# Optimization experiments

Hardware: AMD Instinct MI355X
Metric: run time of the kernel (lower is better)

The kernel has to match this reference:

```python
import jax, jax.numpy as jnp
import numpy as np

NUM_HEADS = 16
ROPE_BASE = 10000.0


def _rope_cos_sin(seq_len, head_dim, dtype):
    inv_freq = 1.0 / (ROPE_BASE ** (jnp.arange(0, head_dim, 2, dtype=jnp.float32) / head_dim))
    t = jnp.arange(seq_len, dtype=jnp.float32)
    freqs = jnp.einsum('i,j->ij', t, inv_freq)          # [S, hd/2]
    emb = jnp.concatenate([freqs, freqs], axis=-1)      # [S, hd]
    return jnp.cos(emb).astype(dtype), jnp.sin(emb).astype(dtype)


def _rotate_half(x):
    x1, x2 = jnp.split(x, 2, axis=-1)
    return jnp.concatenate([-x2, x1], axis=-1)


def setup_inputs() -> dict:
    key = jax.random.key(0)
    k1, k2, k3 = jax.random.split(key, 3)
    B, S, D = 2, 2048, 2048
    x = jax.random.normal(k1, (B, S, D), dtype=jnp.float32)
    w_qkv = jax.random.normal(k2, (D, 3 * D), dtype=jnp.float32) * (D ** -0.5)
    w_out = jax.random.normal(k3, (D, D), dtype=jnp.float32) * (D ** -0.5)
    return {"x": x, "w_qkv": w_qkv, "w_out": w_out}


def reference(x, w_qkv, w_out):
    B, S, D = x.shape
    H = NUM_HEADS
    hd = D // H
    scale = hd ** -0.5

    qkv = jnp.einsum('bsd,de->bse', x, w_qkv)            # [B,S,3D]
    q, k, v = jnp.split(qkv, 3, axis=-1)
    # -> [B,H,S,hd]
    q = q.reshape(B, S, H, hd).transpose(0, 2, 1, 3)
    k = k.reshape(B, S, H, hd).transpose(0, 2, 1, 3)
    v = v.reshape(B, S, H, hd).transpose(0, 2, 1, 3)

    cos, sin = _rope_cos_sin(S, hd, x.dtype)             # [S,hd]
    cos = cos[None, None]                                # [1,1,S,hd]
    sin = sin[None, None]
    q = q * cos + _rotate_half(q) * sin
    k = k * cos + _rotate_half(k) * sin

    scores = jnp.einsum('bhqd,bhkd->bhqk', q, k) * scale  # [B,H,S,S]
    attn = jax.nn.softmax(scores, axis=-1)                # non-causal: no mask
    out = jnp.einsum('bhqk,bhkd->bhqd', attn, v)          # [B,H,S,hd]
    out = out.transpose(0, 2, 1, 3).reshape(B, S, D)
    out = jnp.einsum('bsd,de->bse', out, w_out)
    return out
```

## Files before the change

### kernel.cpp

```cpp
#include <hip/hip_runtime.h>
#include <hip/hip_bf16.h>

typedef __hip_bfloat16 bf16_t;
typedef __bf16 bf16x8 __attribute__((ext_vector_type(8)));
typedef float floatx4 __attribute__((ext_vector_type(4)));

#define DEVINL __device__ __forceinline__

DEVINL floatx4 mfma16(bf16x8 a, bf16x8 b, floatx4 c) {
  return __builtin_amdgcn_mfma_f32_16x16x32_bf16(a, b, c, 0, 0, 0);
}

DEVINL void gload_lds16(const bf16_t* gp, bf16_t* lp) {
  __builtin_amdgcn_global_load_lds(
      (const __attribute__((address_space(1))) unsigned int*)gp,
      (__attribute__((address_space(3))) unsigned int*)lp, 16, 0, 0);
}

template <class CT> DEVINL CT cvtC(float f);
template <> DEVINL bf16_t cvtC<bf16_t>(float f) { return __float2bfloat16(f); }
template <> DEVINL float cvtC<float>(float f) { return f; }

DEVINL unsigned int pack_bf2(float a, float b) {
  union { bf16_t h; unsigned short s; } ua, ub;
  ua.h = __float2bfloat16(a);
  ub.h = __float2bfloat16(b);
  return (unsigned int)ua.s | ((unsigned int)ub.s << 16);
}

__global__ void convert_f32_bf16(const float* __restrict__ in,
                                 bf16_t* __restrict__ out) {
  size_t i = ((size_t)blockIdx.x * 256 + threadIdx.x) * 8;
  floatx4 a = *(const floatx4*)(in + i);
  floatx4 b = *(const floatx4*)(in + i + 4);
  bf16x8 r;
#pragma unroll
  for (int j = 0; j < 4; j++) r[j] = (__bf16)a[j];
#pragma unroll
  for (int j = 0; j < 4; j++) r[4 + j] = (__bf16)b[j];
  *(bf16x8*)(out + i) = r;
}

template <bool SPLITV, class CT>
__global__ __launch_bounds__(256, 3) void gemm_bt(
    const bf16_t* __restrict__ A, const bf16_t* __restrict__ BT,
    CT* __restrict__ C, bf16_t* __restrict__ VTout, int M, int N, int CN,
    int K) {
  __shared__ __align__(16) bf16_t a_lds[8 * 1024];
  __shared__ __align__(16) bf16_t b_lds[8 * 1024];

  const int tid = threadIdx.x;
  const int wave = tid >> 6;
  const int lane = tid & 63;
  const int quad = lane >> 4;
  const int l16 = lane & 15;
  const int wm = wave >> 1, wn = wave & 1;

  const int nx = N >> 7;
  const int bid = blockIdx.x;
  const int row0 = ((bid & 7) + 8 * (bid / (8 * nx))) * 128;
  const int col0 = ((bid >> 3) % nx) * 128;

  floatx4 acc[4][4] = {};

  const bf16_t* ag = A + (size_t)(row0 + wave * 32 + l16) * K + quad * 8;
  const bf16_t* bg = BT + (size_t)(col0 + wave * 32 + l16) * K + quad * 8;

  bf16x8 pa[2][2], pb[2][2];
#define LOAD_TILE(k0)                                                       \
  {                                                                         \
    _Pragma("unroll") for (int t = 0; t < 2; t++)                           \
        _Pragma("unroll") for (int kc = 0; kc < 2; kc++) {                  \
      pa[t][kc] = *(const bf16x8*)(ag + (k0) + (size_t)(t * 16) * K + kc * 32); \
      pb[t][kc] = *(const bf16x8*)(bg + (k0) + (size_t)(t * 16) * K + kc * 32); \
    }                                                                       \
  }
#define STORE_TILE()                                                        \
  {                                                                         \
    _Pragma("unroll") for (int t = 0; t < 2; t++)                           \
        _Pragma("unroll") for (int kc = 0; kc < 2; kc++) {                  \
      *(bf16x8*)(a_lds + (wave * 2 + t) * 1024 + kc * 512 + lane * 8) =     \
          pa[t][kc];                                                        \
      *(bf16x8*)(b_lds + (wave * 2 + t) * 1024 + kc * 512 + lane * 8) =     \
          pb[t][kc];                                                        \
    }                                                                       \
  }

  LOAD_TILE(0);
  STORE_TILE();
  __syncthreads();

  for (int k0 = 0; k0 < K; k0 += 64) {
    const bool more = (k0 + 64) < K;
    if (more) LOAD_TILE(k0 + 64);
#pragma unroll
    for (int kc = 0; kc < 2; kc++) {
      bf16x8 af[4], bfr[4];
#pragma unroll
      for (int i = 0; i < 4; i++)
        af[i] = *(const bf16x8*)(a_lds + (wm * 4 + i) * 1024 + kc * 512 +
                                 lane * 8);
#pragma unroll
      for (int j = 0; j < 4; j++)
        bfr[j] = *(const bf16x8*)(b_lds + (wn * 4 + j) * 1024 + kc * 512 +
                                  lane * 8);
#pragma unroll
      for (int i = 0; i < 4; i++)
#pragma unroll
        for (int j = 0; j < 4; j++)
          acc[i][j] = mfma16(af[i], bfr[j], acc[i][j]);
    }
    __syncthreads();
    if (more) STORE_TILE();
    __syncthreads();
  }
#undef LOAD_TILE
#undef STORE_TILE

  if (!SPLITV || col0 < 4096) {
#pragma unroll
    for (int i = 0; i < 4; i++)
#pragma unroll
      for (int j = 0; j < 4; j++)
#pragma unroll
        for (int r = 0; r < 4; r++) {
          int row = row0 + wm * 64 + i * 16 + quad * 4 + r;
          int col = col0 + wn * 64 + j * 16 + l16;
          C[(size_t)row * CN + col] = cvtC<CT>(acc[i][j][r]);
        }
  } else {
    const int h = (col0 - 4096) >> 7;
    const int b = row0 >> 11;
    const int s0 = row0 & 2047;
    bf16_t* vt = VTout + (size_t)(b * 16 + h) * 128 * 2048;
    struct __align__(8) bf4 { bf16_t v[4]; };
#pragma unroll
    for (int i = 0; i < 4; i++)
#pragma unroll
      for (int j = 0; j < 4; j++) {
        int d = wn * 64 + j * 16 + l16;
        int s = s0 + wm * 64 + i * 16 + quad * 4;
        bf4 o;
#pragma unroll
        for (int r = 0; r < 4; r++) o.v[r] = __float2bfloat16(acc[i][j][r]);
        *(bf4*)(vt + (size_t)d * 2048 + s) = o;
      }
  }
}

__global__ void transposecvt(const float* __restrict__ in,
                             bf16_t* __restrict__ out, int M, int N) {
  __shared__ bf16_t tile[32][33];
  int n0 = blockIdx.x * 32, m0 = blockIdx.y * 32;
  tile[threadIdx.y][threadIdx.x] =
      __float2bfloat16(in[(size_t)(m0 + threadIdx.y) * N + n0 + threadIdx.x]);
  __syncthreads();
  out[(size_t)(n0 + threadIdx.y) * M + m0 + threadIdx.x] =
      tile[threadIdx.x][threadIdx.y];
}

__global__ void rope_qk(bf16_t* __restrict__ qkv) {
  struct __align__(8) bf4 { bf16_t v[4]; };
  int t = blockIdx.x * 256 + threadIdx.x;
  int dc = t & 15;
  int s = (t >> 4) & 2047;
  int h = (t >> 15) & 15;
  int b = t >> 19;
  int d = dc * 4;
  size_t base = ((size_t)(b * 2048 + s) * 2) * 2048 + h * 128;
  bf4 ql = *(const bf4*)(qkv + base + d);
  bf4 qh = *(const bf4*)(qkv + base + d + 64);
  bf4 kl = *(const bf4*)(qkv + base + 2048 + d);
  bf4 kh = *(const bf4*)(qkv + base + 2048 + d + 64);
  bf4 oql, oqh, okl, okh;
  const float scale = 0.08838834764831845f;
#pragma unroll
  for (int i = 0; i < 4; i++) {
    int j = d + i;
    float fr = (float)s * exp2f((float)j * -0.20762050593045858f);
    float c, sn;
    __sincosf(fr, &sn, &c);
    float qlo = __bfloat162float(ql.v[i]), qhi = __bfloat162float(qh.v[i]);
    float klo = __bfloat162float(kl.v[i]), khi = __bfloat162float(kh.v[i]);
    oql.v[i] = __float2bfloat16((qlo * c - qhi * sn) * scale);
    oqh.v[i] = __float2bfloat16((qhi * c + qlo * sn) * scale);
    okl.v[i] = __float2bfloat16(klo * c - khi * sn);
    okh.v[i] = __float2bfloat16(khi * c + klo * sn);
  }
  *(bf4*)(qkv + base + d) = oql;
  *(bf4*)(qkv + base + d + 64) = oqh;
  *(bf4*)(qkv + base + 2048 + d) = okl;
  *(bf4*)(qkv + base + 2048 + d + 64) = okh;
}

__global__ __launch_bounds__(256, 2) void flash_attn(
    const bf16_t* __restrict__ qkv, const bf16_t* __restrict__ VT,
    bf16_t* __restrict__ Out) {
  const int S = 2048;
  const int RS = 4096;
  const int tid = threadIdx.x;
  const int wave = tid >> 6;
  const int lane = tid & 63;
  const int quad = lane >> 4;
  const int l16 = lane & 15;

  const int bh = blockIdx.y;
  const int q0 = blockIdx.x * 128;
  const int b = bh >> 4, h = bh & 15;

  const bf16_t* Qb = qkv + (size_t)b * S * RS + h * 128;
  const bf16_t* Kb = Qb + 2048;
  const bf16_t* Vb = VT + (size_t)bh * 128 * S;

  __shared__ __align__(16) bf16_t k_lds[16384];
  __shared__ __align__(16) bf16_t v_lds[16384];

  bf16x8 qf[2][4];
#pragma unroll
  for (int qn = 0; qn < 2; qn++)
#pragma unroll
    for (int ks = 0; ks < 4; ks++)
      qf[qn][ks] = *(const bf16x8*)(
          Qb + (size_t)(q0 + wave * 32 + qn * 16 + l16) * RS + ks * 32 +
          quad * 8);

  floatx4 o_acc[2][8] = {};
  float l_part[2] = {0.f, 0.f};

  const int sA = l16 + 32 * (quad & 1);
  const int sB = sA + 16;
  const bool hi = quad >= 2;

  for (int kt = 0; kt < S / 128; kt++) {
    const int kk0 = kt * 128;
#pragma unroll
    for (int t = 0; t < 2; t++) {
      int mt = wave * 2 + t;
#pragma unroll
      for (int ks = 0; ks < 4; ks++) {
        gload_lds16(Kb + (size_t)(kk0 + mt * 16 + l16) * RS + ks * 32 + quad * 8,
                    k_lds + mt * 2048 + ks * 512);
        gload_lds16(Vb + (size_t)(mt * 16 + l16) * S + kk0 + ks * 32 + quad * 8,
                    v_lds + mt * 2048 + ks * 512);
      }
    }
    __syncthreads();

    floatx4 s_acc[2][8] = {};
    __builtin_amdgcn_s_setprio(1);
#pragma unroll
    for (int ks = 0; ks < 4; ks++)
#pragma unroll
      for (int mt = 0; mt < 8; mt++) {
        bf16x8 kf = *(const bf16x8*)(k_lds + mt * 2048 + ks * 512 + lane * 8);
        s_acc[0][mt] = mfma16(kf, qf[0][ks], s_acc[0][mt]);
        s_acc[1][mt] = mfma16(kf, qf[1][ks], s_acc[1][mt]);
      }
    __builtin_amdgcn_s_setprio(0);

    unsigned int p01[2][8], p23[2][8];
#pragma unroll
    for (int qn = 0; qn < 2; qn++)
#pragma unroll
      for (int mt = 0; mt < 8; mt++) {
        float e0 = __expf(s_acc[qn][mt][0]);
        float e1 = __expf(s_acc[qn][mt][1]);
        float e2 = __expf(s_acc[qn][mt][2]);
        float e3 = __expf(s_acc[qn][mt][3]);
        l_part[qn] += (e0 + e1) + (e2 + e3);
        p01[qn][mt] = pack_bf2(e0, e1);
        p23[qn][mt] = pack_bf2(e2, e3);
      }

#pragma unroll
    for (int kc = 0; kc < 4; kc++) {
      bf16x8 vf[8];
#pragma unroll
      for (int dt = 0; dt < 8; dt++)
        vf[dt] = *(const bf16x8*)(v_lds + dt * 2048 + kc * 512 + lane * 8);
#pragma unroll
      for (int qn = 0; qn < 2; qn++) {
        unsigned int a0 = __shfl(p01[qn][2 * kc], sA);
        unsigned int b0 = __shfl(p01[qn][2 * kc + 1], sA);
        unsigned int a1 = __shfl(p23[qn][2 * kc], sA);
        unsigned int b1 = __shfl(p23[qn][2 * kc + 1], sA);
        unsigned int a2 = __shfl(p01[qn][2 * kc], sB);
        unsigned int b2 = __shfl(p01[qn][2 * kc + 1], sB);
        unsigned int a3 = __shfl(p23[qn][2 * kc], sB);
        unsigned int b3 = __shfl(p23[qn][2 * kc + 1], sB);
        union { unsigned int u[4]; bf16x8 v; } bp;
        bp.u[0] = hi ? b0 : a0;
        bp.u[1] = hi ? b1 : a1;
        bp.u[2] = hi ? b2 : a2;
        bp.u[3] = hi ? b3 : a3;
        __builtin_amdgcn_s_setprio(1);
#pragma unroll
        for (int dt = 0; dt < 8; dt++)
          o_acc[qn][dt] = mfma16(vf[dt], bp.v, o_acc[qn][dt]);
        __builtin_amdgcn_s_setprio(0);
      }
    }
    __syncthreads();
  }

#pragma unroll
  for (int qn = 0; qn < 2; qn++) {
    l_part[qn] += __shfl_xor(l_part[qn], 16);
    l_part[qn] += __shfl_xor(l_part[qn], 32);
  }

  struct __align__(8) bf4 { bf16_t v[4]; };
#pragma unroll
  for (int qn = 0; qn < 2; qn++) {
    float inv = 1.f / l_part[qn];
    size_t s = q0 + wave * 32 + qn * 16 + l16;
#pragma unroll
    for (int dt = 0; dt < 8; dt++) {
      bf4 o;
#pragma unroll
      for (int r = 0; r < 4; r++)
        o.v[r] = __float2bfloat16(o_acc[qn][dt][r] * inv);
      *(bf4*)(Out + ((size_t)b * S + s) * 2048 + h * 128 + dt * 16 + quad * 4) = o;
    }
  }
}

extern "C" void kernel_launch(void* const* d_in, const int* in_sizes, int n_in,
                              void* d_out, int out_size, void* d_ws,
                              size_t ws_size, hipStream_t stream) {
  const float* x = (const float*)d_in[0];
  const float* w_qkv = (const float*)d_in[1];
  const float* w_out = (const float*)d_in[2];
  float* out = (float*)d_out;
  char* ws = (char*)d_ws;

  const int B = 2, S = 2048, D = 2048;
  bf16_t* qkv2 = (bf16_t*)(ws);
  bf16_t* wqkvT = (bf16_t*)(ws + (size_t)B * S * 2 * D * 2);
  bf16_t* xbf = (bf16_t*)(ws + (size_t)B * S * 2 * D * 2 + (size_t)3 * D * D * 2);
  bf16_t* VT = (bf16_t*)(ws + (size_t)B * S * 2 * D * 2 + (size_t)3 * D * D * 2 +
                         (size_t)B * S * D * 2);
  bf16_t* attn = wqkvT;
  bf16_t* woutT = qkv2;

  dim3 b32(32, 32);
  convert_f32_bf16<<<(B * S * D) / 2048, 256, 0, stream>>>(x, xbf);
  transposecvt<<<dim3(3 * D / 32, D / 32), b32, 0, stream>>>(w_qkv, wqkvT, D, 3 * D);
  gemm_bt<true, bf16_t><<<(B * S / 128) * (3 * D / 128), 256, 0, stream>>>(
      xbf, wqkvT, qkv2, VT, B * S, 3 * D, 2 * D, D);
  rope_qk<<<4096, 256, 0, stream>>>(qkv2);
  flash_attn<<<dim3(S / 128, B * 16), 256, 0, stream>>>(qkv2, VT, attn);
  transposecvt<<<dim3(D / 32, D / 32), b32, 0, stream>>>(w_out, woutT, D, D);
  gemm_bt<false, float><<<(B * S / 128) * (D / 128), 256, 0, stream>>>(
      attn, woutT, out, nullptr, B * S, D, D, D);
}
```

Baseline: 500.7 us.

## Add 256x256-tile 8-wave GEMM with double-buffered LDS pipeline for QKV projection

```diff
diff --git a/kernel.cpp b/kernel.cpp
--- a/kernel.cpp
+++ b/kernel.cpp
@@ -39,6 +39,162 @@
 #pragma unroll
   for (int j = 0; j < 4; j++) r[4 + j] = (__bf16)b[j];
   *(bf16x8*)(out + i) = r;
+}
+
+template <bool SPLITV, class CT>
+__global__ __launch_bounds__(512, 2) void gemm256(
+    const bf16_t* __restrict__ A, const bf16_t* __restrict__ BT,
+    CT* __restrict__ C, bf16_t* __restrict__ VTout, int M, int N, int CN,
+    int K) {
+  extern __shared__ __align__(16) char smem[];
+  bf16_t* a_lds = (bf16_t*)smem;
+  bf16_t* b_lds = a_lds + 32768;
+
+  const int tid = threadIdx.x;
+  const int w = tid >> 6;
+  const int lane = tid & 63;
+  const int quad = lane >> 4;
+  const int l16 = lane & 15;
+  const int wm = w >> 2, wn = w & 3;
+
+  const int cpx = (int)gridDim.x >> 3;
+  const int wgid = ((int)blockIdx.x & 7) * cpx + ((int)blockIdx.x >> 3);
+  const int nym = M >> 8;
+  const int row0 = (wgid % nym) * 256;
+  const int col0 = (wgid / nym) * 256;
+
+  floatx4 acc[2][2][4][2] = {};
+  bf16x8 af[4][2], bfr[2][2];
+
+  const bf16_t* agA = A + (size_t)(row0 + w * 16 + l16) * K + quad * 8;
+  const bf16_t* agB = BT + (size_t)(col0 + w * 16 + l16) * K + quad * 8;
+  const size_t rK = (size_t)128 * K;
+
+#define STG_A(bb, rp, tt)                                                  \
+  {                                                                        \
+    _Pragma("unroll") for (int kc = 0; kc < 2; kc++)                       \
+        gload_lds16(agA + (rp) * rK + (tt) * 64 + kc * 32,                 \
+                    a_lds + (bb) * 16384 + ((rp) * 8 + w) * 1024 + kc * 512); \
+  }
+#define STG_B(bb, cp, tt)                                                  \
+  {                                                                        \
+    _Pragma("unroll") for (int kc = 0; kc < 2; kc++)                       \
+        gload_lds16(agB + (cp) * rK + (tt) * 64 + kc * 32,                 \
+                    b_lds + (bb) * 16384 + ((cp) * 8 + w) * 1024 + kc * 512); \
+  }
+#define LDA(cb, rp)                                                        \
+  {                                                                        \
+    _Pragma("unroll") for (int m = 0; m < 4; m++)                          \
+        _Pragma("unroll") for (int kc = 0; kc < 2; kc++)                   \
+            af[m][kc] = *(const bf16x8*)(a_lds + (cb) * 16384 +            \
+                                         ((rp) * 8 + wm * 4 + m) * 1024 +  \
+                                         kc * 512 + lane * 8);             \
+  }
+#define LDB(cb, cp)                                                        \
+  {                                                                        \
+    _Pragma("unroll") for (int n = 0; n < 2; n++)                          \
+        _Pragma("unroll") for (int kc = 0; kc < 2; kc++)                   \
+            bfr[n][kc] = *(const bf16x8*)(b_lds + (cb) * 16384 +           \
+                                          ((cp) * 8 + wn * 2 + n) * 1024 + \
+                                          kc * 512 + lane * 8);            \
+  }
+#define MM(rp, cp)                                                         \
+  {                                                                        \
+    __builtin_amdgcn_s_setprio(1);                                         \
+    _Pragma("unroll") for (int kc = 0; kc < 2; kc++)                       \
+        _Pragma("unroll") for (int m = 0; m < 4; m++)                      \
+            _Pragma("unroll") for (int n = 0; n < 2; n++)                  \
+                acc[rp][cp][m][n] =                                        \
+                    mfma16(af[m][kc], bfr[n][kc], acc[rp][cp][m][n]);      \
+    __builtin_amdgcn_s_setprio(0);                                         \
+  }
+#define BAR()                         \
+  {                                   \
+    __builtin_amdgcn_s_barrier();     \
+    __builtin_amdgcn_sched_barrier(0); \
+  }
+#define VM(n)                                              \
+  {                                                        \
+    asm volatile("s_waitcnt vmcnt(" #n ")" ::: "memory");  \
+    __builtin_amdgcn_sched_barrier(0);                     \
+  }
+
+#define TILE(tt, cb, nb, DOSTG, V0m, V1m, V3m)             \
+  {                                                        \
+     LDA(cb, 0); LDB(cb, 0);                         \
+    if (DOSTG) { STG_A(nb, 0, (tt) + 1); STG_B(nb, 0, (tt) + 1); } \
+    V0m BAR(); MM(0, 0); BAR();                            \
+     LDB(cb, 1);                                     \
+    if (DOSTG) STG_B(nb, 1, (tt) + 1);                     \
+    V1m BAR(); MM(0, 1); BAR();                            \
+     LDA(cb, 1);                                     \
+    if (DOSTG) STG_A(nb, 1, (tt) + 1);                     \
+    BAR(); MM(1, 1); BAR();                                \
+     LDB(cb, 0);                                     \
+    V3m BAR(); MM(1, 0); BAR();                            \
+  }
+
+  STG_A(0, 0, 0); STG_B(0, 0, 0); STG_B(0, 1, 0); STG_A(0, 1, 0);
+  VM(4);
+  __builtin_amdgcn_s_barrier();
+  __builtin_amdgcn_sched_barrier(0);
+
+  const int nt = K >> 6;
+  for (int t = 0; t < nt - 2; t += 2) {
+    TILE(t, 0, 1, 1, VM(6);, VM(6);, VM(4);)
+    TILE(t + 1, 1, 0, 1, VM(6);, VM(6);, VM(4);)
+  }
+  TILE(nt - 2, 0, 1, 1, VM(6);, VM(6);, VM(4);)
+  TILE(nt - 1, 1, 0, 0, VM(2);, VM(0);, )
+
+#undef TILE
+#undef VM
+#undef BAR
+#undef MM
+#undef LDB
+#undef LDA
+#undef STG_B
+#undef STG_A
+
+  if (!SPLITV || col0 < 4096) {
+#pragma unroll
+    for (int rp = 0; rp < 2; rp++)
+#pragma unroll
+      for (int cp = 0; cp < 2; cp++)
+#pragma unroll
+        for (int m = 0; m < 4; m++)
+#pragma unroll
+          for (int n = 0; n < 2; n++)
+#pragma unroll
+            for (int r = 0; r < 4; r++) {
+              int row = row0 + rp * 128 + wm * 64 + m * 16 + quad * 4 + r;
+              int col = col0 + cp * 128 + wn * 32 + n * 16 + l16;
+              C[(size_t)row * CN + col] = cvtC<CT>(acc[rp][cp][m][n][r]);
+            }
+  } else {
+    const int b = row0 >> 11;
+    const int s0 = row0 & 2047;
+    struct __align__(8) bf4 { bf16_t v[4]; };
+#pragma unroll
+    for (int cp = 0; cp < 2; cp++) {
+      const int h = ((col0 - 4096) >> 7) + cp;
+      bf16_t* vt = VTout + (size_t)(b * 16 + h) * 128 * 2048;
+#pragma unroll
+      for (int rp = 0; rp < 2; rp++)
+#pragma unroll
+        for (int m = 0; m < 4; m++)
+#pragma unroll
+          for (int n = 0; n < 2; n++) {
+            int d = wn * 32 + n * 16 + l16;
+            int s = s0 + rp * 128 + wm * 64 + m * 16 + quad * 4;
+            bf4 o;
+#pragma unroll
+            for (int r = 0; r < 4; r++)
+              o.v[r] = __float2bfloat16(acc[rp][cp][m][n][r]);
+            *(bf4*)(vt + (size_t)d * 2048 + s) = o;
+          }
+    }
+  }
 }
 
 template <bool SPLITV, class CT>
@@ -343,10 +499,13 @@
   bf16_t* attn = wqkvT;
   bf16_t* woutT = qkv2;
 
+  hipFuncSetAttribute(reinterpret_cast<const void*>(&gemm256<true, bf16_t>),
+                      hipFuncAttributeMaxDynamicSharedMemorySize, 131072);
+
   dim3 b32(32, 32);
   convert_f32_bf16<<<(B * S * D) / 2048, 256, 0, stream>>>(x, xbf);
   transposecvt<<<dim3(3 * D / 32, D / 32), b32, 0, stream>>>(w_qkv, wqkvT, D, 3 * D);
-  gemm_bt<true, bf16_t><<<(B * S / 128) * (3 * D / 128), 256, 0, stream>>>(
+  gemm256<true, bf16_t><<<(B * S / 256) * (3 * D / 256), 512, 131072, stream>>>(
       xbf, wqkvT, qkv2, VT, B * S, 3 * D, 2 * D, D);
   rope_qk<<<4096, 256, 0, stream>>>(qkv2);
   flash_attn<<<dim3(S / 128, B * 16), 256, 0, stream>>>(qkv2, VT, attn);
```

Result: faster. 450.7 us (-10.0%).

## Rewrite GEMM as 128x256 tile with triple-buffered direct-to-LDS loads

Applied to the files above, without the earlier changes.

```diff
diff --git a/kernel.cpp b/kernel.cpp
--- a/kernel.cpp
+++ b/kernel.cpp
@@ -42,107 +42,150 @@
 }
 
 template <bool SPLITV, class CT>
-__global__ __launch_bounds__(256, 3) void gemm_bt(
+__global__ __launch_bounds__(512, 2) void gemm128(
     const bf16_t* __restrict__ A, const bf16_t* __restrict__ BT,
     CT* __restrict__ C, bf16_t* __restrict__ VTout, int M, int N, int CN,
     int K) {
-  __shared__ __align__(16) bf16_t a_lds[8 * 1024];
-  __shared__ __align__(16) bf16_t b_lds[8 * 1024];
+  extern __shared__ __align__(16) char smem[];
+  bf16_t* a_lds = (bf16_t*)smem;
+  bf16_t* b_lds = a_lds + 24576;
 
   const int tid = threadIdx.x;
-  const int wave = tid >> 6;
+  const int w = tid >> 6;
   const int lane = tid & 63;
   const int quad = lane >> 4;
   const int l16 = lane & 15;
-  const int wm = wave >> 1, wn = wave & 1;
-
-  const int nx = N >> 7;
-  const int bid = blockIdx.x;
-  const int row0 = ((bid & 7) + 8 * (bid / (8 * nx))) * 128;
-  const int col0 = ((bid >> 3) % nx) * 128;
+  const int wm = w >> 2, wn = w & 3;
+
+  const int cpx = (int)gridDim.x >> 3;
+  const int wgid = ((int)blockIdx.x & 7) * cpx + ((int)blockIdx.x >> 3);
+  const int nym = M >> 7;
+  const int row0 = (wgid % nym) * 128;
+  const int col0 = (wgid / nym) * 256;
 
   floatx4 acc[4][4] = {};
-
-  const bf16_t* ag = A + (size_t)(row0 + wave * 32 + l16) * K + quad * 8;
-  const bf16_t* bg = BT + (size_t)(col0 + wave * 32 + l16) * K + quad * 8;
-
-  bf16x8 pa[2][2], pb[2][2];
-#define LOAD_TILE(k0)                                                       \
-  {                                                                         \
-    _Pragma("unroll") for (int t = 0; t < 2; t++)                           \
-        _Pragma("unroll") for (int kc = 0; kc < 2; kc++) {                  \
-      pa[t][kc] = *(const bf16x8*)(ag + (k0) + (size_t)(t * 16) * K + kc * 32); \
-      pb[t][kc] = *(const bf16x8*)(bg + (k0) + (size_t)(t * 16) * K + kc * 32); \
-    }                                                                       \
-  }
-#define STORE_TILE()                                                        \
-  {                                                                         \
-    _Pragma("unroll") for (int t = 0; t < 2; t++)                           \
-        _Pragma("unroll") for (int kc = 0; kc < 2; kc++) {                  \
-      *(bf16x8*)(a_lds + (wave * 2 + t) * 1024 + kc * 512 + lane * 8) =     \
-          pa[t][kc];                                                        \
-      *(bf16x8*)(b_lds + (wave * 2 + t) * 1024 + kc * 512 + lane * 8) =     \
-          pb[t][kc];                                                        \
-    }                                                                       \
-  }
-
-  LOAD_TILE(0);
-  STORE_TILE();
-  __syncthreads();
-
-  for (int k0 = 0; k0 < K; k0 += 64) {
-    const bool more = (k0 + 64) < K;
-    if (more) LOAD_TILE(k0 + 64);
-#pragma unroll
-    for (int kc = 0; kc < 2; kc++) {
-      bf16x8 af[4], bfr[4];
-#pragma unroll
-      for (int i = 0; i < 4; i++)
-        af[i] = *(const bf16x8*)(a_lds + (wm * 4 + i) * 1024 + kc * 512 +
-                                 lane * 8);
-#pragma unroll
-      for (int j = 0; j < 4; j++)
-        bfr[j] = *(const bf16x8*)(b_lds + (wn * 4 + j) * 1024 + kc * 512 +
-                                  lane * 8);
-#pragma unroll
-      for (int i = 0; i < 4; i++)
-#pragma unroll
-        for (int j = 0; j < 4; j++)
-          acc[i][j] = mfma16(af[i], bfr[j], acc[i][j]);
-    }
-    __syncthreads();
-    if (more) STORE_TILE();
-    __syncthreads();
-  }
-#undef LOAD_TILE
-#undef STORE_TILE
+  bf16x8 af[4][2], bfr[2][2];
+
+  const int nfE = (w >> 1) * 4 + (w & 1);
+  const bf16_t* agA = A + (size_t)(row0 + w * 16 + l16) * K + quad * 8;
+  const bf16_t* agB = BT + (size_t)(col0 + nfE * 16 + l16) * K + quad * 8;
+
+#define STG_A(sb, tt)                                                      \
+  {                                                                        \
+    _Pragma("unroll") for (int kc = 0; kc < 2; kc++)                       \
+        gload_lds16(agA + (tt) * 64 + kc * 32,                             \
+                    a_lds + (sb) * 8192 + w * 1024 + kc * 512);            \
+  }
+#define STG_BE(sb, tt)                                                     \
+  {                                                                        \
+    _Pragma("unroll") for (int kc = 0; kc < 2; kc++)                       \
+        gload_lds16(agB + (tt) * 64 + kc * 32,                             \
+                    b_lds + (sb) * 16384 + nfE * 1024 + kc * 512);         \
+  }
+#define STG_BO(sb, tt)                                                     \
+  {                                                                        \
+    _Pragma("unroll") for (int kc = 0; kc < 2; kc++)                       \
+        gload_lds16(agB + (size_t)32 * K + (tt) * 64 + kc * 32,            \
+                    b_lds + (sb) * 16384 + (nfE + 2) * 1024 + kc * 512);   \
+  }
+#define LDA(cb)                                                            \
+  {                                                                        \
+    _Pragma("unroll") for (int m = 0; m < 4; m++)                          \
+        _Pragma("unroll") for (int kc = 0; kc < 2; kc++)                   \
+            af[m][kc] = *(const bf16x8*)(a_lds + (cb) * 8192 +             \
+                                         (wm * 4 + m) * 1024 + kc * 512 +  \
+                                         lane * 8);                        \
+  }
+#define LDB(cb, h)                                                         \
+  {                                                                        \
+    _Pragma("unroll") for (int jj = 0; jj < 2; jj++)                       \
+        _Pragma("unroll") for (int kc = 0; kc < 2; kc++)                   \
+            bfr[jj][kc] = *(const bf16x8*)(b_lds + (cb) * 16384 +          \
+                                           (wn * 4 + 2 * (h) + jj) * 1024 + \
+                                           kc * 512 + lane * 8);           \
+  }
+#define MM(h)                                                              \
+  {                                                                        \
+    __builtin_amdgcn_s_setprio(1);                                         \
+    _Pragma("unroll") for (int kc = 0; kc < 2; kc++)                       \
+        _Pragma("unroll") for (int m = 0; m < 4; m++)                      \
+            _Pragma("unroll") for (int jj = 0; jj < 2; jj++)               \
+                acc[m][2 * (h) + jj] = mfma16(af[m][kc], bfr[jj][kc],      \
+                                              acc[m][2 * (h) + jj]);       \
+    __builtin_amdgcn_s_setprio(0);                                         \
+  }
+#define BAR()                          \
+  {                                    \
+    __builtin_amdgcn_s_barrier();      \
+    __builtin_amdgcn_sched_barrier(0); \
+  }
+#define VM(n)                                              \
+  {                                                        \
+    asm volatile("s_waitcnt vmcnt(" #n ")" ::: "memory");  \
+    __builtin_amdgcn_sched_barrier(0);                     \
+  }
+
+#define TILE(tt, cb, sb, DOSTG, V0m, V1m)                  \
+  {                                                        \
+     LDA(cb); LDB(cb, 0);                            \
+    if (DOSTG) { STG_A(sb, (tt) + 2); STG_BE(sb, (tt) + 2); } \
+    V0m BAR(); MM(0); BAR();                               \
+     LDB(cb, 1);                                     \
+    if (DOSTG) { STG_BO(sb, (tt) + 2); }                   \
+    V1m BAR(); MM(1); BAR();                               \
+  }
+
+  STG_A(0, 0); STG_BE(0, 0); STG_BO(0, 0);
+  STG_A(1, 1); STG_BE(1, 1); STG_BO(1, 1);
+  VM(8);
+  __builtin_amdgcn_s_barrier();
+  __builtin_amdgcn_sched_barrier(0);
+
+  const int nt = K >> 6;
+  for (int t = 0; t < nt - 2; t += 3) {
+    TILE(t, 0, 2, 1, VM(10);, VM(8);)
+    TILE(t + 1, 1, 0, 1, VM(10);, VM(8);)
+    TILE(t + 2, 2, 1, 1, VM(10);, VM(8);)
+  }
+  TILE(nt - 2, 0, 0, 0, VM(6);, VM(2);)
+  TILE(nt - 1, 1, 0, 0, VM(0);, )
+
+#undef TILE
+#undef VM
+#undef BAR
+#undef MM
+#undef LDB
+#undef LDA
+#undef STG_BO
+#undef STG_BE
+#undef STG_A
 
   if (!SPLITV || col0 < 4096) {
 #pragma unroll
-    for (int i = 0; i < 4; i++)
-#pragma unroll
-      for (int j = 0; j < 4; j++)
+    for (int m = 0; m < 4; m++)
+#pragma unroll
+      for (int n = 0; n < 4; n++)
 #pragma unroll
         for (int r = 0; r < 4; r++) {
-          int row = row0 + wm * 64 + i * 16 + quad * 4 + r;
-          int col = col0 + wn * 64 + j * 16 + l16;
-          C[(size_t)row * CN + col] = cvtC<CT>(acc[i][j][r]);
+          int row = row0 + wm * 64 + m * 16 + quad * 4 + r;
+          int col = col0 + wn * 64 + n * 16 + l16;
+          C[(size_t)row * CN + col] = cvtC<CT>(acc[m][n][r]);
         }
   } else {
-    const int h = (col0 - 4096) >> 7;
     const int b = row0 >> 11;
     const int s0 = row0 & 2047;
+    const int h = ((col0 - 4096) >> 7) + (wn >> 1);
     bf16_t* vt = VTout + (size_t)(b * 16 + h) * 128 * 2048;
     struct __align__(8) bf4 { bf16_t v[4]; };
 #pragma unroll
-    for (int i = 0; i < 4; i++)
-#pragma unroll
-      for (int j = 0; j < 4; j++) {
-        int d = wn * 64 + j * 16 + l16;
-        int s = s0 + wm * 64 + i * 16 + quad * 4;
+    for (int m = 0; m < 4; m++)
+#pragma unroll
+      for (int n = 0; n < 4; n++) {
+        int d = (wn & 1) * 64 + n * 16 + l16;
+        int s = s0 + wm * 64 + m * 16 + quad * 4;
         bf4 o;
 #pragma unroll
-        for (int r = 0; r < 4; r++) o.v[r] = __float2bfloat16(acc[i][j][r]);
+        for (int r = 0; r < 4; r++) o.v[r] = __float2bfloat16(acc[m][n][r]);
         *(bf4*)(vt + (size_t)d * 2048 + s) = o;
       }
   }
@@ -343,14 +386,19 @@
   bf16_t* attn = wqkvT;
   bf16_t* woutT = qkv2;
 
+  hipFuncSetAttribute(reinterpret_cast<const void*>(&gemm128<true, bf16_t>),
+                      hipFuncAttributeMaxDynamicSharedMemorySize, 147456);
+  hipFuncSetAttribute(reinterpret_cast<const void*>(&gemm128<false, float>),
+                      hipFuncAttributeMaxDynamicSharedMemorySize, 147456);
+
   dim3 b32(32, 32);
   convert_f32_bf16<<<(B * S * D) / 2048, 256, 0, stream>>>(x, xbf);
   transposecvt<<<dim3(3 * D / 32, D / 32), b32, 0, stream>>>(w_qkv, wqkvT, D, 3 * D);
-  gemm_bt<true, bf16_t><<<(B * S / 128) * (3 * D / 128), 256, 0, stream>>>(
+  gemm128<true, bf16_t><<<(B * S / 128) * (3 * D / 256), 512, 147456, stream>>>(
       xbf, wqkvT, qkv2, VT, B * S, 3 * D, 2 * D, D);
   rope_qk<<<4096, 256, 0, stream>>>(qkv2);
   flash_attn<<<dim3(S / 128, B * 16), 256, 0, stream>>>(qkv2, VT, attn);
   transposecvt<<<dim3(D / 32, D / 32), b32, 0, stream>>>(w_out, woutT, D, D);
-  gemm_bt<false, float><<<(B * S / 128) * (D / 128), 256, 0, stream>>>(
+  gemm128<false, float><<<(B * S / 128) * (D / 256), 512, 147456, stream>>>(
       attn, woutT, out, nullptr, B * S, D, D, D);
 }
```

Result: faster. 448.0 us (-10.5%).
